# Optimization experiments

Measured on AMD Instinct MI355X. Metric: run time of the kernel, lower is better.

Reference implementation:

```python
import jax, jax.numpy as jnp
import numpy as np

B, T, A, K, STEPS, E = 2, 16384, 128, 128, 16, 126


def soft_dirac_last(x):
    # softmax forward-replaced by one-hot(argmax), straight-through backward
    sm = jax.nn.softmax(x, axis=-1)
    hard = jax.nn.one_hot(jnp.argmax(x, axis=-1), x.shape[-1], dtype=x.dtype)
    return sm + jax.lax.stop_gradient(hard - sm)


def _encode(x, d_unit, atom_embeddings):
    # x: (B,1,T); d_unit: (A,K) unit-norm atoms
    rng = jnp.linspace(0.0, 1.0, T, dtype=x.dtype)
    kernel = d_unit[:, None, :]  # OIH
    pad = [(K // 2, K - 1 - K // 2)]  # SAME
    batch_ix = jnp.arange(B)

    def step(res, _):
        # dense feature map: correlation of residual with every atom
        fm = jax.lax.conv_general_dilated(
            res, kernel, window_strides=(1,), padding=pad,
            dimension_numbers=("NCH", "OIH", "NCH"))  # (B,A,T)
        flat = fm.reshape(B, A * T)
        fi = jnp.argmax(flat, axis=-1)                      # sparsify n_to_keep=1
        value = jnp.take_along_axis(flat, fi[:, None], axis=-1)  # (B,1)
        ai = fi // T
        ti = fi % T
        # position: soft_dirac over time of sparse fm summed over atoms
        pos_row = jnp.zeros((B, T), x.dtype).at[batch_ix, ti].set(value[:, 0])
        pd = soft_dirac_last(pos_row)
        position = jnp.sum(pd * rng[None, :], axis=-1, keepdims=True) * 20.0  # (B,1)
        # atom one-hot: soft_dirac over atom axis of sparse fm summed over time
        atom_row = jnp.zeros((B, A), x.dtype).at[batch_ix, ai].set(value[:, 0])
        ad = soft_dirac_last(atom_row)
        ae = ad @ atom_embeddings  # (B,E)
        emb = jnp.concatenate([position, value, ae], axis=-1)  # (B, 2+E)
        # matching-pursuit residual update: subtract value * atom at found shift
        recon = value * d_unit[ai]  # (B,K)
        buf = jnp.zeros((B, T + K), x.dtype)
        buf = jax.vmap(lambda bb, rr, tt: jax.lax.dynamic_update_slice(bb, rr, (tt,)))(buf, recon, ti)
        res = res - buf[:, None, K // 2:K // 2 + T]
        return res, emb

    res, embs = jax.lax.scan(step, x, None, length=STEPS)
    embs = jnp.transpose(embs, (1, 0, 2))  # (B, STEPS, 2+E)
    return embs, res


def _canonical_ordering(embs, proj):
    keys = embs @ proj  # (B, STEPS)
    order = jnp.argsort(keys, axis=-1)
    return jnp.take_along_axis(embs, order[:, :, None], axis=1)


def setup_inputs() -> dict:
    key = jax.random.key(0)
    ks = jax.random.split(key, 5)
    return {
        "a": jax.random.normal(ks[0], (B, 1, T), jnp.float32),
        "b": jax.random.normal(ks[1], (B, 1, T), jnp.float32),
        "d": jax.random.normal(ks[2], (A, K), jnp.float32),
        "atom_embeddings": jax.random.normal(ks[3], (A, E), jnp.float32) * 0.1,
        "ordering_proj": jax.random.normal(ks[4], (128,), jnp.float32),
    }


def reference(a, b, d, atom_embeddings, ordering_proj):
    d_unit = d / (jnp.linalg.norm(d, axis=-1, keepdims=True) + 1e-8)
    ae, a_res = _encode(a, d_unit, atom_embeddings)
    be, b_res = _encode(b, d_unit, atom_embeddings)
    ae = _canonical_ordering(ae, ordering_proj)
    be = _canonical_ordering(be, ordering_proj)
    a_norm = jnp.linalg.norm(a_res.reshape(-1, T), axis=-1)
    b_norm = jnp.linalg.norm(b_res.reshape(-1, T), axis=-1)
    return jnp.mean((ae - be) ** 2) + jnp.mean(jnp.abs(a_norm - b_norm))
```

## Files before the change

kernel.cpp:

```cpp
#include <hip/hip_runtime.h>
#include <math.h>

#define T_DIM 16384
#define A_DIM 128
#define K_DIM 128
#define N_STEPS 16
#define E_DIM 126
#define NSEQ 4

#define ATI 16
#define TT 256
#define NTT 64
#define NPT 512
#define INC_B 16
#define RS_PAD 392

__device__ inline unsigned long long pack_vi(float v, int fi) {
    unsigned int b = __float_as_uint(v);
    b = (b & 0x80000000u) ? ~b : (b | 0x80000000u);
    return ((unsigned long long)b << 32) | (unsigned int)(~fi);
}
__device__ inline void unpack_vi(unsigned long long p, float* v, int* fi) {
    unsigned int lo = (unsigned int)(p & 0xffffffffu);
    unsigned int b = (unsigned int)(p >> 32);
    unsigned int fb = (b & 0x80000000u) ? (b & 0x7fffffffu) : ~b;
    *v = __uint_as_float(fb);
    *fi = (int)(~lo);
}

__global__ __launch_bounds__(256) void k_prep(
    const float* __restrict__ d, const float* __restrict__ a,
    const float* __restrict__ b, float* __restrict__ du,
    float* __restrict__ res, int* __restrict__ cnt,
    unsigned long long* __restrict__ slots) {
    int blk = blockIdx.x, tid = threadIdx.x;
    if (blk < 128) {
        __shared__ float s[128];
        float v = 0.0f;
        if (tid < 128) { v = d[blk * K_DIM + tid]; s[tid] = v * v; }
        __syncthreads();
        for (int off = 64; off > 0; off >>= 1) {
            if (tid < off) s[tid] += s[tid + off];
            __syncthreads();
        }
        if (tid < 128) du[blk * K_DIM + tid] = v / (sqrtf(s[0]) + 1e-8f);
    } else if (blk < 384) {
        int i = (blk - 128) * 256 + tid;
        res[i] = (i < 2 * T_DIM) ? a[i] : b[i - 2 * T_DIM];
    } else {
        if (tid < NSEQ) cnt[tid] = 0;
        for (int i = tid; i < (N_STEPS - 1) * NSEQ * INC_B; i += 256) slots[i] = 0ULL;
    }
}

__device__ inline unsigned long long tile_fast(
    const float* __restrict__ res, const float* __restrict__ du,
    int seq, int a_base, int t0, int tid,
    float* res_sh, float* rv_sh, int* ri_sh,
    const float* val_h, const int* ti_h, const int* ai_h, int nh) {

    const float* resS = res + seq * T_DIM;
    for (int i = tid; i < RS_PAD; i += 256) {
        int t = t0 + i - K_DIM / 2;
        float v = 0.0f;
        if (t >= 0 && t < T_DIM && i < TT + K_DIM - 1) {
            v = resS[t];
            for (int s = 0; s < nh; s++) {
                int dk = t - (ti_h[s] - K_DIM / 2);
                if (dk >= 0 && dk < K_DIM)
                    v = __fsub_rn(v, __fmul_rn(val_h[s], du[ai_h[s] * K_DIM + dk]));
            }
        }
        res_sh[i] = v;
    }
    __syncthreads();

    int tg = tid & 63;
    int ag = __builtin_amdgcn_readfirstlane(tid >> 6);
    const float* duP = du + (a_base + ag * 4) * K_DIM;

    float acc[4][4];
    #pragma unroll
    for (int i = 0; i < 4; i++)
        #pragma unroll
        for (int j = 0; j < 4; j++) acc[i][j] = 0.0f;

    float r[8];
    *(float4*)&r[0] = *(const float4*)&res_sh[4 * tg];
    *(float4*)&r[4] = *(const float4*)&res_sh[4 * tg + 4];

    #pragma unroll 4
    for (int k = 0; k < K_DIM; k += 4) {
        float dA[4][4];
        #pragma unroll
        for (int i = 0; i < 4; i++)
            *(float4*)dA[i] = *(const float4*)(duP + i * K_DIM + k);
        #pragma unroll
        for (int dk = 0; dk < 4; dk++) {
            #pragma unroll
            for (int i = 0; i < 4; i++) {
                float s = dA[i][dk];
                #pragma unroll
                for (int j = 0; j < 4; j++)
                    acc[i][j] = fmaf(s, r[j + dk], acc[i][j]);
            }
        }
        r[0] = r[4]; r[1] = r[5]; r[2] = r[6]; r[3] = r[7];
        *(float4*)&r[4] = *(const float4*)&res_sh[4 * tg + k + 8];
    }

    float bv = -INFINITY;
    int bi = 0x7fffffff;
    #pragma unroll
    for (int i = 0; i < 4; i++) {
        int a = a_base + ag * 4 + i;
        #pragma unroll
        for (int j = 0; j < 4; j++) {
            int t = t0 + 4 * tg + j;
            int fi = a * T_DIM + t;
            float v = acc[i][j];
            if (v > bv || (v == bv && fi < bi)) { bv = v; bi = fi; }
        }
    }
    rv_sh[tid] = bv;
    ri_sh[tid] = bi;
    __syncthreads();
    for (int off = 128; off > 0; off >>= 1) {
        if (tid < off) {
            float v2 = rv_sh[tid + off]; int i2 = ri_sh[tid + off];
            if (v2 > rv_sh[tid] || (v2 == rv_sh[tid] && i2 < ri_sh[tid])) {
                rv_sh[tid] = v2; ri_sh[tid] = i2;
            }
        }
        __syncthreads();
    }
    return pack_vi(rv_sh[0], ri_sh[0]);
}

__global__ __launch_bounds__(256) void k_step_full(
    float* __restrict__ res, const float* __restrict__ du,
    const float* __restrict__ ae, float* __restrict__ emb,
    unsigned long long* __restrict__ pmax, int* __restrict__ cnt,
    int* __restrict__ dirty0) {

    int seq = blockIdx.y;
    int blk = blockIdx.x;
    int a_base = (blk >> 6) * ATI;
    int t0 = (blk & 63) * TT;
    int tid = threadIdx.x;

    alignas(16) __shared__ float res_sh[RS_PAD];
    __shared__ float rv_sh[256];
    __shared__ int   ri_sh[256];
    __shared__ unsigned long long pm_sh[256];
    __shared__ int last_flag;

    unsigned long long p = tile_fast(res, du, seq, a_base, t0, tid,
                                     res_sh, rv_sh, ri_sh,
                                     nullptr, nullptr, nullptr, 0);
    if (tid == 0) {
        pmax[seq * NPT + blk] = p;
        __threadfence();
        last_flag = (atomicAdd(&cnt[seq], 1) == NPT - 1);
    }
    __syncthreads();
    if (!last_flag) return;

    __threadfence();
    {
        unsigned long long m0 = pmax[seq * NPT + tid];
        unsigned long long m1 = pmax[seq * NPT + 256 + tid];
        pm_sh[tid] = m0 > m1 ? m0 : m1;
    }
    __syncthreads();
    for (int off = 128; off > 0; off >>= 1) {
        if (tid < off) { if (pm_sh[tid + off] > pm_sh[tid]) pm_sh[tid] = pm_sh[tid + off]; }
        __syncthreads();
    }
    float value; int fi;
    unpack_vi(pm_sh[0], &value, &fi);
    int ai = fi >> 14;
    int ti = fi & (T_DIM - 1);
    int pos_idx = value > 0.0f ? ti : 0;
    int atom_idx = value > 0.0f ? ai : 0;

    float* e = emb + (seq * N_STEPS + 0) * 128;
    if (tid == 0) {
        e[0] = ((float)pos_idx / (float)(T_DIM - 1)) * 20.0f;
        e[1] = value;
        int nlo = ti - (K_DIM - 1); if (nlo < 0) nlo = 0;
        int nhi = ti + K_DIM;       if (nhi > T_DIM) nhi = T_DIM;
        dirty0[seq * 2 + 0] = nlo;
        dirty0[seq * 2 + 1] = nhi;
    }
    if (tid >= 2 && tid < 2 + E_DIM) e[tid] = ae[atom_idx * E_DIM + tid - 2];
    if (tid >= 128) {
        int k = tid - 128;
        int t = ti + k - K_DIM / 2;
        if (t >= 0 && t < T_DIM) {
            float r = res[seq * T_DIM + t];
            res[seq * T_DIM + t] = __fsub_rn(r, __fmul_rn(value, du[ai * K_DIM + k]));
        }
    }
}

__global__ __launch_bounds__(256) void k_inc(
    float* __restrict__ res, const float* __restrict__ du,
    const float* __restrict__ ae, float* __restrict__ emb,
    const unsigned long long* __restrict__ pmax,
    unsigned long long* __restrict__ slots, const int* __restrict__ dirty0) {

    int seq = blockIdx.y;
    int blk = blockIdx.x;
    int atile = blk >> 1;
    int par = blk & 1;
    int a_base = atile * ATI;
    int tid = threadIdx.x;

    alignas(16) __shared__ float res_sh[RS_PAD];
    __shared__ float rv_sh[256];
    __shared__ int   ri_sh[256];
    __shared__ unsigned long long tmax[32];
    __shared__ unsigned long long poll_sh[INC_B];
    __shared__ float val_h[N_STEPS - 1];
    __shared__ int   ti_h[N_STEPS - 1];
    __shared__ int   ai_h[N_STEPS - 1];
    __shared__ int   lo_sh, hi_sh;

    if (tid < 32) tmax[tid] = pmax[seq * NPT + atile * NTT + par + 2 * tid];
    int lo = dirty0[seq * 2 + 0];
    int hi = dirty0[seq * 2 + 1];
    __syncthreads();

    for (int step = 1; step < N_STEPS; step++) {
        int T0 = lo >> 8;
        int tt = ((T0 & 1) == par) ? T0 : T0 + 1;
        bool valid = (tt < NTT) && (tt * TT < hi);

        if (valid) {
            unsigned long long p = tile_fast(res, du, seq, a_base, tt * TT,
                                             tid, res_sh, rv_sh, ri_sh,
                                             val_h, ti_h, ai_h, step - 1);
            if (tid == 0) tmax[(tt - par) >> 1] = p;
        }
        if (tid == 0) {
            unsigned long long m = tmax[0];
            for (int j = 1; j < 32; j++) if (tmax[j] > m) m = tmax[j];
            atomicExch(&slots[((step - 1) * NSEQ + seq) * INC_B + blk], m);
        }
        if (tid < INC_B) {
            unsigned long long* sp = &slots[((step - 1) * NSEQ + seq) * INC_B + tid];
            unsigned long long v = atomicAdd(sp, 0ULL);
            while (v == 0ULL) { __builtin_amdgcn_s_sleep(2); v = atomicAdd(sp, 0ULL); }
            poll_sh[tid] = v;
        }
        __syncthreads();
        if (tid == 0) {
            unsigned long long w = poll_sh[0];
            for (int j = 1; j < INC_B; j++) if (poll_sh[j] > w) w = poll_sh[j];
            float value; int fi;
            unpack_vi(w, &value, &fi);
            int ti = fi & (T_DIM - 1);
            val_h[step - 1] = value;
            ti_h[step - 1] = ti;
            ai_h[step - 1] = fi >> 14;
            int nlo = ti - (K_DIM - 1); if (nlo < 0) nlo = 0;
            int nhi = ti + K_DIM;       if (nhi > T_DIM) nhi = T_DIM;
            lo_sh = nlo; hi_sh = nhi;
        }
        __syncthreads();

        if (blk == 0) {
            float value = val_h[step - 1];
            int ti = ti_h[step - 1], ai = ai_h[step - 1];
            int pos_idx = value > 0.0f ? ti : 0;
            int atom_idx = value > 0.0f ? ai : 0;
            float* e = emb + (seq * N_STEPS + step) * 128;
            if (tid == 0) {
                e[0] = ((float)pos_idx / (float)(T_DIM - 1)) * 20.0f;
                e[1] = value;
            }
            if (tid >= 2 && tid < 128) e[tid] = ae[atom_idx * E_DIM + tid - 2];
        }
        lo = lo_sh; hi = hi_sh;
    }

    if (blk == 0) {
        __syncthreads();
        for (int s = 0; s < N_STEPS - 1; s++) {
            if (tid < 128) {
                int t = ti_h[s] - K_DIM / 2 + tid;
                if (t >= 0 && t < T_DIM) {
                    float r = res[seq * T_DIM + t];
                    res[seq * T_DIM + t] =
                        __fsub_rn(r, __fmul_rn(val_h[s], du[ai_h[s] * K_DIM + tid]));
                }
            }
            __syncthreads();
        }
    }
}

__global__ __launch_bounds__(1024) void k_tail(
    const float* __restrict__ res, const float* __restrict__ emb,
    const float* __restrict__ proj, float* __restrict__ out) {
    int tid = threadIdx.x;
    __shared__ float sh[1024];
    __shared__ float norms[NSEQ];
    __shared__ float keys[NSEQ][N_STEPS];
    __shared__ int   order[NSEQ][N_STEPS];

    {
        int seq = tid >> 8;
        int ln  = tid & 255;
        const float4* r4 = (const float4*)(res + seq * T_DIM);
        float s = 0.0f;
        #pragma unroll
        for (int j = 0; j < 16; j++) {
            float4 v = r4[j * 256 + ln];
            s = fmaf(v.x, v.x, s); s = fmaf(v.y, v.y, s);
            s = fmaf(v.z, v.z, s); s = fmaf(v.w, v.w, s);
        }
        sh[tid] = s;
        __syncthreads();
        for (int off = 128; off > 0; off >>= 1) {
            if (ln < off) sh[tid] += sh[tid + off];
            __syncthreads();
        }
        if (ln == 0) norms[seq] = sqrtf(sh[tid]);
        __syncthreads();
    }
    {
        int pair = tid >> 4;
        int seq = pair >> 4, st = pair & 15;
        int ln = tid & 15;
        const float* e = emb + (seq * N_STEPS + st) * 128 + ln * 8;
        const float* pr = proj + ln * 8;
        float kk = 0.0f;
        #pragma unroll
        for (int dd = 0; dd < 8; dd++) kk = fmaf(e[dd], pr[dd], kk);
        sh[tid] = kk;
        __syncthreads();
        for (int off = 8; off > 0; off >>= 1) {
            if (ln < off) sh[tid] += sh[tid + off];
            __syncthreads();
        }
        if (ln == 0) keys[seq][st] = sh[tid];
        __syncthreads();
    }
    if (tid < NSEQ) {
        int ord[N_STEPS];
        for (int i = 0; i < N_STEPS; i++) ord[i] = i;
        for (int i = 1; i < N_STEPS; i++) {
            int oi = ord[i];
            float kv = keys[tid][oi];
            int j = i - 1;
            while (j >= 0 && keys[tid][ord[j]] > kv) { ord[j + 1] = ord[j]; j--; }
            ord[j + 1] = oi;
        }
        for (int i = 0; i < N_STEPS; i++) order[tid][i] = ord[i];
    }
    __syncthreads();
    float s = 0.0f;
    #pragma unroll
    for (int t = 0; t < 4; t++) {
        int idx = tid + t * 1024;
        int b  = idx >> 11;
        int st = (idx >> 7) & 15;
        int dd = idx & 127;
        float va = emb[((b    ) * N_STEPS + order[b    ][st]) * 128 + dd];
        float vb = emb[((2 + b) * N_STEPS + order[2 + b][st]) * 128 + dd];
        float df = va - vb;
        s = fmaf(df, df, s);
    }
    sh[tid] = s;
    __syncthreads();
    for (int off = 512; off > 0; off >>= 1) {
        if (tid < off) sh[tid] += sh[tid + off];
        __syncthreads();
    }
    if (tid == 0) {
        float mse = sh[0] / 4096.0f;
        float mad = 0.5f * (fabsf(norms[0] - norms[2]) + fabsf(norms[1] - norms[3]));
        out[0] = mse + mad;
    }
}

extern "C" void kernel_launch(void* const* d_in, const int* in_sizes, int n_in,
                              void* d_out, int out_size, void* d_ws, size_t ws_size,
                              hipStream_t stream) {
    const float* a    = (const float*)d_in[0];
    const float* b    = (const float*)d_in[1];
    const float* d    = (const float*)d_in[2];
    const float* ae   = (const float*)d_in[3];
    const float* proj = (const float*)d_in[4];
    float* out = (float*)d_out;

    float* ws  = (float*)d_ws;
    float* res = ws;
    float* du  = res + NSEQ * T_DIM;
    float* emb = du + A_DIM * K_DIM;
    unsigned long long* pmax  = (unsigned long long*)(emb + NSEQ * N_STEPS * 128);
    unsigned long long* slots = pmax + NSEQ * NPT;
    int* cnt    = (int*)(slots + (N_STEPS - 1) * NSEQ * INC_B);
    int* dirty0 = cnt + NSEQ;

    k_prep<<<385, 256, 0, stream>>>(d, a, b, du, res, cnt, slots);

    dim3 gfull(NPT, NSEQ);
    k_step_full<<<gfull, 256, 0, stream>>>(res, du, ae, emb, pmax, cnt, dirty0);

    dim3 ginc(INC_B, NSEQ);
    k_inc<<<ginc, 256, 0, stream>>>(res, du, ae, emb, pmax, slots, dirty0);

    k_tail<<<1, 1024, 0, stream>>>(res, emb, proj, out);
}
```

Baseline: 260.5 us.

## Use wavefront shuffle argmax reduction and atomic-load polling in matching-pursuit tiles

Replaces the 8-round shared-memory tree argmax, which needs a barrier per round, with a 64-lane wavefront shuffle reduction followed by a 4-entry shared combine of packed value/index keys. The spin-wait on cross-block slots now uses relaxed agent-scope atomic loads with a shorter sleep instead of atomicAdd(0) read-modify-writes. It also splits the shared residual float4 loads into float2 loads, probably to avoid LDS bank conflicts or misaligned accesses. The aim is fewer barriers and less atomic traffic on the latency-bound per-step critical path.

Result: faster. 252.1 us (-3.2%).

```diff
diff --git a/kernel.cpp b/kernel.cpp
--- a/kernel.cpp
+++ b/kernel.cpp
@@ -56,7 +56,7 @@
 __device__ inline unsigned long long tile_fast(
     const float* __restrict__ res, const float* __restrict__ du,
     int seq, int a_base, int t0, int tid,
-    float* res_sh, float* rv_sh, int* ri_sh,
+    float* res_sh, unsigned long long* red4,
     const float* val_h, const int* ti_h, const int* ai_h, int nh) {
 
     const float* resS = res + seq * T_DIM;
@@ -86,8 +86,10 @@
         for (int j = 0; j < 4; j++) acc[i][j] = 0.0f;
 
     float r[8];
-    *(float4*)&r[0] = *(const float4*)&res_sh[4 * tg];
-    *(float4*)&r[4] = *(const float4*)&res_sh[4 * tg + 4];
+    *(float2*)&r[0] = *(const float2*)&res_sh[4 * tg + 0];
+    *(float2*)&r[2] = *(const float2*)&res_sh[4 * tg + 2];
+    *(float2*)&r[4] = *(const float2*)&res_sh[4 * tg + 4];
+    *(float2*)&r[6] = *(const float2*)&res_sh[4 * tg + 6];
 
     #pragma unroll 4
     for (int k = 0; k < K_DIM; k += 4) {
@@ -106,7 +108,8 @@
             }
         }
         r[0] = r[4]; r[1] = r[5]; r[2] = r[6]; r[3] = r[7];
-        *(float4*)&r[4] = *(const float4*)&res_sh[4 * tg + k + 8];
+        *(float2*)&r[4] = *(const float2*)&res_sh[4 * tg + k + 8];
+        *(float2*)&r[6] = *(const float2*)&res_sh[4 * tg + k + 10];
     }
 
     float bv = -INFINITY;
@@ -122,19 +125,22 @@
             if (v > bv || (v == bv && fi < bi)) { bv = v; bi = fi; }
         }
     }
-    rv_sh[tid] = bv;
-    ri_sh[tid] = bi;
-    __syncthreads();
-    for (int off = 128; off > 0; off >>= 1) {
-        if (tid < off) {
-            float v2 = rv_sh[tid + off]; int i2 = ri_sh[tid + off];
-            if (v2 > rv_sh[tid] || (v2 == rv_sh[tid] && i2 < ri_sh[tid])) {
-                rv_sh[tid] = v2; ri_sh[tid] = i2;
-            }
-        }
-        __syncthreads();
-    }
-    return pack_vi(rv_sh[0], ri_sh[0]);
+    #pragma unroll
+    for (int off = 32; off > 0; off >>= 1) {
+        float v2 = __shfl_down(bv, off);
+        int   i2 = __shfl_down(bi, off);
+        if (v2 > bv || (v2 == bv && i2 < bi)) { bv = v2; bi = i2; }
+    }
+    if ((tid & 63) == 0) red4[tid >> 6] = pack_vi(bv, bi);
+    __syncthreads();
+    if (tid == 0) {
+        unsigned long long m = red4[0];
+        #pragma unroll
+        for (int w = 1; w < 4; w++) if (red4[w] > m) m = red4[w];
+        red4[0] = m;
+    }
+    __syncthreads();
+    return red4[0];
 }
 
 __global__ __launch_bounds__(256) void k_step_full(
@@ -150,14 +156,12 @@
     int tid = threadIdx.x;
 
     alignas(16) __shared__ float res_sh[RS_PAD];
-    __shared__ float rv_sh[256];
-    __shared__ int   ri_sh[256];
+    __shared__ unsigned long long red4[4];
     __shared__ unsigned long long pm_sh[256];
     __shared__ int last_flag;
 
     unsigned long long p = tile_fast(res, du, seq, a_base, t0, tid,
-                                     res_sh, rv_sh, ri_sh,
-                                     nullptr, nullptr, nullptr, 0);
+                                     res_sh, red4, nullptr, nullptr, nullptr, 0);
     if (tid == 0) {
         pmax[seq * NPT + blk] = p;
         __threadfence();
@@ -218,8 +222,7 @@
     int tid = threadIdx.x;
 
     alignas(16) __shared__ float res_sh[RS_PAD];
-    __shared__ float rv_sh[256];
-    __shared__ int   ri_sh[256];
+    __shared__ unsigned long long red4[4];
     __shared__ unsigned long long tmax[32];
     __shared__ unsigned long long poll_sh[INC_B];
     __shared__ float val_h[N_STEPS - 1];
@@ -239,7 +242,7 @@
 
         if (valid) {
             unsigned long long p = tile_fast(res, du, seq, a_base, tt * TT,
-                                             tid, res_sh, rv_sh, ri_sh,
+                                             tid, res_sh, red4,
                                              val_h, ti_h, ai_h, step - 1);
             if (tid == 0) tmax[(tt - par) >> 1] = p;
         }
@@ -249,9 +252,15 @@
             atomicExch(&slots[((step - 1) * NSEQ + seq) * INC_B + blk], m);
         }
         if (tid < INC_B) {
-            unsigned long long* sp = &slots[((step - 1) * NSEQ + seq) * INC_B + tid];
-            unsigned long long v = atomicAdd(sp, 0ULL);
-            while (v == 0ULL) { __builtin_amdgcn_s_sleep(2); v = atomicAdd(sp, 0ULL); }
+            const unsigned long long* sp =
+                &slots[((step - 1) * NSEQ + seq) * INC_B + tid];
+            unsigned long long v = __hip_atomic_load(sp, __ATOMIC_RELAXED,
+                                                     __HIP_MEMORY_SCOPE_AGENT);
+            while (v == 0ULL) {
+                __builtin_amdgcn_s_sleep(1);
+                v = __hip_atomic_load(sp, __ATOMIC_RELAXED,
+                                      __HIP_MEMORY_SCOPE_AGENT);
+            }
             poll_sh[tid] = v;
         }
         __syncthreads();
```
